# Optimization experiments

Measured on AMD Instinct MI355X. Metric: run time of the kernel, lower is better.

## Reference

```python
import jax, jax.numpy as jnp
import numpy as np

BN_EPS = 1e-5


def setup_inputs() -> dict:
    key = jax.random.key(0)
    ks = jax.random.split(key, 11)
    B, C, Ci, D, H, W = 2, 256, 128, 8, 32, 32
    s = 0.02  # weight init scale
    return {
        "x": jax.random.normal(ks[0], (B, C, D, H, W), dtype=jnp.float32),
        "Wt": jax.random.normal(ks[1], (Ci, C), dtype=jnp.float32) * s,
        "bt": jax.random.normal(ks[2], (Ci,), dtype=jnp.float32) * s,
        "Wp": jax.random.normal(ks[3], (Ci, C), dtype=jnp.float32) * s,
        "bp": jax.random.normal(ks[4], (Ci,), dtype=jnp.float32) * s,
        "Wg": jax.random.normal(ks[5], (Ci, C), dtype=jnp.float32) * s,
        "bg": jax.random.normal(ks[6], (Ci,), dtype=jnp.float32) * s,
        "Ww": jax.random.normal(ks[7], (C, Ci), dtype=jnp.float32) * s,
        "bw": jax.random.normal(ks[8], (C,), dtype=jnp.float32) * s,
        "gamma": jax.random.normal(ks[9], (C,), dtype=jnp.float32),
        "beta": jax.random.normal(ks[10], (C,), dtype=jnp.float32),
    }


def reference(x, Wt, bt, Wp, bp, Wg, bg, Ww, bw, gamma, beta):
    # x: [B, C, D, H, W]; 1x1x1 Conv3d == per-position channel GEMM.
    B, C, D, H, W = x.shape
    xf = x.reshape(B, C, -1)  # [B, C, N], N = D*H*W

    theta = jnp.einsum('oc,bcn->bno', Wt, xf) + bt          # [B, N, Ci]
    phi = jnp.einsum('oc,bcn->bon', Wp, xf) + bp[None, :, None]  # [B, Ci, N]
    g = jnp.einsum('oc,bcn->bno', Wg, xf) + bg              # [B, N, Ci]

    # Unscaled, unmasked full self-attention over all N spatial positions.
    f = jnp.einsum('bnc,bcm->bnm', theta, phi)              # [B, N, N]
    a = jax.nn.softmax(f, axis=-1)
    y = jnp.einsum('bnm,bmc->bcn', a, g)                    # [B, Ci, N]

    # Output projection W: conv1x1 then BatchNorm3d (training-mode batch stats).
    wy = jnp.einsum('oc,bcn->bon', Ww, y) + bw[None, :, None]  # [B, C, N]
    mean = jnp.mean(wy, axis=(0, 2), keepdims=True)
    var = jnp.var(wy, axis=(0, 2), keepdims=True)
    wy_bn = (wy - mean) * jax.lax.rsqrt(var + BN_EPS)
    wy_bn = wy_bn * gamma[None, :, None] + beta[None, :, None]

    return wy_bn.reshape(B, C, D, H, W) + x
```

## Files before the change

### kernel.cpp

```cpp
#include <hip/hip_runtime.h>
#include <cstdint>
#include <cstddef>


typedef unsigned short u16;
typedef __bf16 bf16x8 __attribute__((ext_vector_type(8)));
typedef float f32x4 __attribute__((ext_vector_type(4)));
typedef float f32x16 __attribute__((ext_vector_type(16)));
typedef unsigned short u16x8 __attribute__((ext_vector_type(8)));

#define B_ 2
#define C_ 256
#define CI_ 128
#define N_ 8192
#define CHUNKS 4
#define CHUNK_N 2048
#define KVB 64
#define NT (CHUNK_N/KVB)

static __device__ __forceinline__ u16 f2bf(float f){
  unsigned u = __builtin_bit_cast(unsigned, f);
  unsigned r = (u + 0x7FFFu + ((u>>16)&1u)) >> 16;
  return (u16)r;
}
static __device__ __forceinline__ float bf2f(u16 v){
  unsigned u = ((unsigned)v) << 16;
  return __builtin_bit_cast(float, u);
}
static __device__ __forceinline__ f32x4 f4zero(){
  f32x4 v; v[0]=0.f; v[1]=0.f; v[2]=0.f; v[3]=0.f; return v;
}
static __device__ __forceinline__ f32x16 f16zero(){
  f32x16 v;
#pragma unroll
  for (int i=0;i<16;i++) v[i]=0.f;
  return v;
}
static __device__ __forceinline__ f32x4 mfma16(bf16x8 a, bf16x8 b, f32x4 c){
  return __builtin_amdgcn_mfma_f32_16x16x32_bf16(a, b, c, 0, 0, 0);
}
static __device__ __forceinline__ f32x16 mfma32(bf16x8 a, bf16x8 b, f32x16 c){
  return __builtin_amdgcn_mfma_f32_32x32x16_bf16(a, b, c, 0, 0, 0);
}
static __device__ __forceinline__ unsigned cvtpk(float lo, float hi){
  unsigned r;
  asm("v_cvt_pk_bf16_f32 %0, %1, %2" : "=v"(r) : "v"(lo), "v"(hi));
  return r;
}
static __device__ __forceinline__ void plswap(unsigned &a, unsigned &b){
  asm volatile("v_permlane32_swap_b32 %0, %1" : "+v"(a), "+v"(b));
}

__global__ void k0_prep(const float* __restrict__ Wt, const float* __restrict__ Wp,
                        const float* __restrict__ Wg, const float* __restrict__ Ww,
                        const float* __restrict__ bt, const float* __restrict__ bp,
                        const float* __restrict__ bg,
                        u16* __restrict__ Wcat, u16* __restrict__ Wwb,
                        float* __restrict__ biasc, float* __restrict__ stats){
  int t = blockIdx.x*blockDim.x + threadIdx.x;
  int nthr = gridDim.x*blockDim.x;
  for (int i = t; i < 32768; i += nthr){
    Wcat[i]        = f2bf(Wt[i]);
    Wcat[32768+i]  = f2bf(Wp[i]);
    Wcat[65536+i]  = f2bf(Wg[i]);
    Wwb[i]         = f2bf(Ww[i]);
  }
  for (int i = t; i < 128; i += nthr){
    biasc[i] = bt[i]; biasc[128+i] = bp[i]; biasc[256+i] = bg[i];
  }
  for (int i = t; i < 512; i += nthr) stats[i] = 0.f;
}

__global__ __launch_bounds__(256) void k1_proj(const float* __restrict__ x,
     const u16* __restrict__ Wcat, const float* __restrict__ biasc,
     u16* __restrict__ theta, u16* __restrict__ kproj, u16* __restrict__ gT){
  __shared__ u16 At[64*264];
  __shared__ u16 Wt_[32*264];
  __shared__ u16 gbuf[32*72];
  int tid = threadIdx.x;
  int b  = blockIdx.x >> 7;
  int nb = (blockIdx.x & 127) * 64;
  int w = tid >> 6, lane = tid & 63;
  int l15 = lane & 15, kg = lane >> 4;

  {
    int cp = tid & 127, nh = tid >> 7;
    int c0 = cp*2;
    const float* src0 = x + ((size_t)(b*C_ + c0))*N_ + nb + nh*32;
    const float* src1 = src0 + N_;
#pragma unroll
    for (int j=0;j<8;j++){
      f32x4 a = *(const f32x4*)(src0 + j*4);
      f32x4 c = *(const f32x4*)(src1 + j*4);
#pragma unroll
      for (int q=0;q<4;q++){
        unsigned pk = (unsigned)f2bf(a[q]) | ((unsigned)f2bf(c[q])<<16);
        *(unsigned*)&At[(nh*32 + j*4 + q)*264 + c0] = pk;
      }
    }
  }
  __syncthreads();

  bf16x8 afr[8];
#pragma unroll
  for (int kc=0;kc<8;kc++)
    afr[kc] = *(const bf16x8*)&At[(w*16+l15)*264 + kc*32 + kg*8];

  for (int och = 0; och < 12; och++){
    {
      int o8 = tid>>3, cp8 = tid&7;
      const u16* wsrc = Wcat + ((size_t)(och*32 + o8))*256 + cp8*8;
#pragma unroll
      for (int j=0;j<4;j++)
        *(u16x8*)&Wt_[o8*264 + cp8*8 + j*64] = *(const u16x8*)(wsrc + j*64);
    }
    __syncthreads();

    f32x4 acc0 = f4zero(), acc1 = f4zero();
#pragma unroll
    for (int kc=0;kc<8;kc++){
      bf16x8 b0 = *(const bf16x8*)&Wt_[(l15)*264 + kc*32 + kg*8];
      bf16x8 b1 = *(const bf16x8*)&Wt_[(16+l15)*264 + kc*32 + kg*8];
      acc0 = mfma16(afr[kc], b0, acc0);
      acc1 = mfma16(afr[kc], b1, acc1);
    }

    if (och < 8){
      u16* dst = (och < 4) ? theta : kproj;
      int oo = (och & 3) * 32;
#pragma unroll
      for (int of=0;of<2;of++){
        int o = oo + of*16 + l15;
        float bias = biasc[och*32 + of*16 + l15];
        f32x4 acc = of ? acc1 : acc0;
#pragma unroll
        for (int i=0;i<4;i++){
          int n = nb + w*16 + kg*4 + i;
          dst[((size_t)b*N_ + n)*CI_ + o] = f2bf(acc[i] + bias);
        }
      }
      __syncthreads();
    } else {
#pragma unroll
      for (int of=0;of<2;of++){
        int o = of*16 + l15;
        float bias = biasc[och*32 + of*16 + l15];
        f32x4 acc = of ? acc1 : acc0;
#pragma unroll
        for (int i=0;i<4;i++){
          int r = w*16 + kg*4 + i;
          gbuf[o*72 + r] = f2bf(acc[i] + bias);
        }
      }
      __syncthreads();
      {
        int o = tid>>3, np = tid&7;
        int og = (och-8)*32 + o;
        u16x8 v = *(const u16x8*)&gbuf[o*72 + np*8];
        *(u16x8*)(gT + ((size_t)b*CI_ + og)*N_ + nb + np*8) = v;
      }
      __syncthreads();
    }
  }
}

__global__ __launch_bounds__(512, 2) void k2_attn(const u16* __restrict__ theta,
      const u16* __restrict__ kproj, const u16* __restrict__ gT,
      u16* __restrict__ pO, float* __restrict__ pM, float* __restrict__ pL){
  __shared__ char smem[65536];
  char* kbase = smem;
  char* vbase = smem + 32768;
  int tid = threadIdx.x;
  int bid = blockIdx.x;
  int combo = bid & 7;
  int b = combo & 1;
  int chunk = combo >> 1;
  int qblk = bid >> 3;
  int n0 = chunk * CHUNK_N;
  int w = tid >> 6, lane = tid & 63;
  int l31 = lane & 31, hi = lane >> 5;
  int qg = qblk*256 + w*32 + l31;

  bf16x8 qf[8];
  {
    const u16* qsrc = theta + ((size_t)b*N_ + qg)*CI_ + hi*8;
#pragma unroll
    for (int cc=0; cc<8; cc++) qf[cc] = *(const bf16x8*)(qsrc + cc*16);
  }

  int krow_s = tid >> 3, kpart = tid & 7;
  int vrow_s = tid >> 2, vpart = tid & 3;
  const u16* ksrc = kproj + ((size_t)b*N_ + n0 + krow_s)*CI_ + kpart*16;
  const u16* vsrc = gT + ((size_t)b*CI_ + vrow_s)*N_ + n0 + vpart*16;
  int kw_off[2], vw_off[2];
#pragma unroll
  for (int j=0;j<2;j++){
    int cb = kpart*32 + j*16;
    kw_off[j] = krow_s*256 + (cb ^ ((krow_s&7)<<4));
    int kb = vpart*32 + j*16;
    vw_off[j] = vrow_s*128 + (kb ^ ((vrow_s&7)<<4));
  }
  int swz = (l31&7)<<4;
  int kro[8], vro[4];
#pragma unroll
  for (int cc=0;cc<8;cc++) kro[cc] = l31*256 + ((cc*32 + hi*16) ^ swz);
#pragma unroll
  for (int ks=0;ks<4;ks++) vro[ks] = l31*128 + ((ks*32 + hi*16) ^ swz);

#pragma unroll
  for (int j=0;j<2;j++){
    *(u16x8*)(kbase + kw_off[j]) = *(const u16x8*)(ksrc + j*8);
    *(u16x8*)(vbase + vw_off[j]) = *(const u16x8*)(vsrc + j*8);
  }
  __syncthreads();

  f32x16 oacc[4];
#pragma unroll
  for (int i=0;i<4;i++) oacc[i] = f16zero();
  float mrun = -1e30f, lrun = 0.f;

  for (int t=0; t<NT; t++){
    int cur = t & 1;
    char* kb_c = kbase + cur*16384;
    char* vb_c = vbase + cur*16384;
    u16x8 kst[2], vst[2];
    bool pf = (t+1 < NT);
    if (pf){
      const u16* ks = ksrc + (size_t)(t+1)*KVB*CI_;
      const u16* vs = vsrc + (t+1)*KVB;
#pragma unroll
      for (int j=0;j<2;j++) kst[j] = *(const u16x8*)(ks + j*8);
#pragma unroll
      for (int j=0;j<2;j++) vst[j] = *(const u16x8*)(vs + j*8);
    }

    f32x16 sA = f16zero(), sB = f16zero();
    __builtin_amdgcn_s_setprio(1);
#pragma unroll
    for (int cc=0; cc<8; cc++){
      bf16x8 kf0 = *(const bf16x8*)(kb_c + kro[cc]);
      bf16x8 kf1 = *(const bf16x8*)(kb_c + 8192 + kro[cc]);
      sA = mfma32(kf0, qf[cc], sA);
      sB = mfma32(kf1, qf[cc], sB);
    }
    __builtin_amdgcn_s_setprio(0);

    float t8[8];
#pragma unroll
    for (int i=0;i<8;i++) t8[i] = fmaxf(fmaxf(sA[i], sA[i+8]), fmaxf(sB[i], sB[i+8]));
    float m4a = fmaxf(t8[0], t8[4]), m4b = fmaxf(t8[1], t8[5]);
    float m4c = fmaxf(t8[2], t8[6]), m4d = fmaxf(t8[3], t8[7]);
    float mx = fmaxf(fmaxf(m4a, m4b), fmaxf(m4c, m4d));
    mx = fmaxf(mx, __shfl_xor(mx, 32));
    if (__any(mx > mrun + 8.f)){
      float mnew = fmaxf(mrun, mx);
      float sc = __expf(mrun - mnew);
      lrun *= sc;
#pragma unroll
      for (int i=0;i<4;i++)
#pragma unroll
        for (int r=0;r<16;r++) oacc[i][r] *= sc;
      mrun = mnew;
    }
    float pA[16], pB[16];
#pragma unroll
    for (int r=0;r<16;r++){ pA[r] = __expf(sA[r]-mrun); pB[r] = __expf(sB[r]-mrun); }
    float s8[8];
#pragma unroll
    for (int i=0;i<8;i++) s8[i] = (pA[i]+pA[i+8]) + (pB[i]+pB[i+8]);
    float s4a = s8[0]+s8[4], s4b = s8[1]+s8[5], s4c = s8[2]+s8[6], s4d = s8[3]+s8[7];
    float ps = (s4a+s4b) + (s4c+s4d);
    ps += __shfl_xor(ps, 32);
    lrun += ps;

    if (pf){
      char* kd = kbase + (cur^1)*16384;
      char* vd = vbase + (cur^1)*16384;
#pragma unroll
      for (int j=0;j<2;j++) *(u16x8*)(kd + kw_off[j]) = kst[j];
#pragma unroll
      for (int j=0;j<2;j++) *(u16x8*)(vd + vw_off[j]) = vst[j];
    }

    __builtin_amdgcn_s_setprio(1);
#pragma unroll
    for (int ks=0; ks<4; ks++){
      const float* P = (ks<2) ? pA : pB;
      int r0 = (ks&1)*8;
      unsigned a0 = cvtpk(P[r0+0], P[r0+1]);
      unsigned b0 = cvtpk(P[r0+4], P[r0+5]);
      unsigned a1 = cvtpk(P[r0+2], P[r0+3]);
      unsigned b1 = cvtpk(P[r0+6], P[r0+7]);
      plswap(a0, b0); plswap(a1, b1);
      union { unsigned u[4]; bf16x8 v; } pb;
      pb.u[0]=a0; pb.u[1]=a1; pb.u[2]=b0; pb.u[3]=b1;
#pragma unroll
      for (int c2=0; c2<4; c2++){
        bf16x8 vf = *(const bf16x8*)(vb_c + c2*4096 + vro[ks]);
        oacc[c2] = mfma32(vf, pb.v, oacc[c2]);
      }
    }
    __builtin_amdgcn_s_setprio(0);
    __syncthreads();
  }

  char* region = smem + w*8192;
#pragma unroll
  for (int c2=0;c2<4;c2++)
#pragma unroll
    for (int r=0;r<16;r++){
      int c = c2*32 + (r&3) + 8*(r>>2) + 4*hi;
      *(u16*)(region + l31*256 + ((c*2) ^ swz)) = f2bf(oacc[c2][r]);
    }
  __syncthreads();
  {
    int ql = lane >> 1, half = lane & 1;
    int qg2 = qblk*256 + w*32 + ql;
    u16* dst = pO + ((size_t)(chunk*2 + b)*N_ + qg2)*CI_ + half*64;
    int rswz = (ql&7)<<4;
#pragma unroll
    for (int j=0;j<8;j++){
      u16x8 v2 = *(const u16x8*)(region + ql*256 + ((half*128 + j*16) ^ rswz));
      *(u16x8*)(dst + j*8) = v2;
    }
  }
  if (hi == 0){
    pM[(size_t)(chunk*2 + b)*N_ + qg] = mrun;
    pL[(size_t)(chunk*2 + b)*N_ + qg] = lrun;
  }
}

__global__ __launch_bounds__(256) void k2b_combine(const u16* __restrict__ pO,
    const float* __restrict__ pM, const float* __restrict__ pL,
    float* __restrict__ y){
  int tid = threadIdx.x;
  int blk = blockIdx.x;
  int b = blk >> 9;
  int q = (blk & 511) * 16 + (tid >> 4);
  int c0 = (tid & 15) * 8;
  size_t qi = (size_t)b*N_ + q;
  float m0 = pM[qi], m1 = pM[2*(size_t)N_ + qi], m2 = pM[4*(size_t)N_ + qi], m3 = pM[6*(size_t)N_ + qi];
  float M = fmaxf(fmaxf(m0,m1), fmaxf(m2,m3));
  float w0 = __expf(m0-M), w1 = __expf(m1-M), w2 = __expf(m2-M), w3 = __expf(m3-M);
  float L = w0*pL[qi] + w1*pL[2*(size_t)N_+qi] + w2*pL[4*(size_t)N_+qi] + w3*pL[6*(size_t)N_+qi];
  float inv = 1.f/L;
  float wts[4] = {w0,w1,w2,w3};
  float acc[8];
#pragma unroll
  for (int i=0;i<8;i++) acc[i]=0.f;
  const u16* src = pO + qi*CI_ + c0;
#pragma unroll
  for (int ch=0; ch<4; ch++){
    u16x8 v = *(const u16x8*)(src + (size_t)ch*2*N_*CI_);
#pragma unroll
    for (int i=0;i<8;i++) acc[i] += wts[ch]*bf2f(v[i]);
  }
  float* dst = y + qi*CI_ + c0;
  f32x4 o0, o1;
#pragma unroll
  for (int i=0;i<4;i++){ o0[i] = acc[i]*inv; o1[i] = acc[4+i]*inv; }
  *(f32x4*)dst = o0;
  *(f32x4*)(dst+4) = o1;
}

__global__ __launch_bounds__(256) void k3_wy(const float* __restrict__ y,
    const u16* __restrict__ Wwb, const float* __restrict__ bw,
    float* __restrict__ wy, float* __restrict__ stats){
  __shared__ u16 Yt[64*136];
  __shared__ u16 Wt_[64*136];
  __shared__ float wyb[64*72];
  int tid = threadIdx.x;
  int b  = blockIdx.x >> 7;
  int nb = (blockIdx.x & 127) * 64;
  int w = tid>>6, lane = tid&63;
  int l15 = lane&15, kg = lane>>4;

  {
    int n = tid>>2, cp = tid&3;
    const float* src = y + ((size_t)b*N_ + nb + n)*CI_ + cp*32;
#pragma unroll
    for (int j=0;j<8;j++){
      f32x4 v = *(const f32x4*)(src + j*4);
      unsigned p0 = (unsigned)f2bf(v[0]) | ((unsigned)f2bf(v[1])<<16);
      unsigned p1 = (unsigned)f2bf(v[2]) | ((unsigned)f2bf(v[3])<<16);
      *(unsigned*)&Yt[n*136 + cp*32 + j*4]     = p0;
      *(unsigned*)&Yt[n*136 + cp*32 + j*4 + 2] = p1;
    }
  }
  __syncthreads();

  bf16x8 afr[4];
#pragma unroll
  for (int kc=0;kc<4;kc++)
    afr[kc] = *(const bf16x8*)&Yt[(w*16+l15)*136 + kc*32 + kg*8];

  for (int oc=0; oc<4; oc++){
    {
      int o = tid>>2, cp = tid&3;
      const u16* src = Wwb + ((size_t)(oc*64 + o))*CI_ + cp*32;
#pragma unroll
      for (int j=0;j<4;j++)
        *(u16x8*)&Wt_[o*136 + cp*32 + j*8] = *(const u16x8*)(src + j*8);
    }
    __syncthreads();

    f32x4 acc[4];
#pragma unroll
    for (int of=0;of<4;of++) acc[of] = f4zero();
#pragma unroll
    for (int kc=0;kc<4;kc++){
#pragma unroll
      for (int of=0;of<4;of++){
        bf16x8 bfr = *(const bf16x8*)&Wt_[(of*16+l15)*136 + kc*32 + kg*8];
        acc[of] = mfma16(afr[kc], bfr, acc[of]);
      }
    }
#pragma unroll
    for (int of=0;of<4;of++){
#pragma unroll
      for (int i=0;i<4;i++)
        wyb[(of*16+l15)*72 + w*16 + kg*4 + i] = acc[of][i];
    }
    __syncthreads();
    {
      int o = tid>>2, np = tid&3;
      int og = oc*64 + o;
      float bias = bw[og];
      float sm = 0.f, sq = 0.f;
      float* dst = wy + ((size_t)b*C_ + og)*N_ + nb + np*16;
#pragma unroll
      for (int j=0;j<4;j++){
        f32x4 v;
#pragma unroll
        for (int q=0;q<4;q++){
          float t2 = wyb[o*72 + np*16 + j*4 + q] + bias;
          v[q] = t2; sm += t2; sq += t2*t2;
        }
        *(f32x4*)(dst + j*4) = v;
      }
      sm += __shfl_xor(sm, 1); sm += __shfl_xor(sm, 2);
      sq += __shfl_xor(sq, 1); sq += __shfl_xor(sq, 2);
      if ((tid&3)==0){
        atomicAdd(&stats[og], sm);
        atomicAdd(&stats[256+og], sq);
      }
    }
    __syncthreads();
  }
}

__global__ __launch_bounds__(256) void k4_bn(const float* __restrict__ wy,
    const float* __restrict__ x, const float* __restrict__ stats,
    const float* __restrict__ gamma, const float* __restrict__ beta,
    float* __restrict__ out){
  size_t base = ((size_t)blockIdx.x)*2048 + (size_t)threadIdx.x*8;
  int o = (int)((base >> 13) & 255);
  const float invn = 1.f/16384.f;
  float mean = stats[o]*invn;
  float var  = stats[256+o]*invn - mean*mean;
  float rs = rsqrtf(var + 1e-5f);
  float g = gamma[o]*rs;
  float bb = beta[o];
  f32x4 a0 = *(const f32x4*)(wy + base);
  f32x4 a1 = *(const f32x4*)(wy + base + 4);
  f32x4 x0 = *(const f32x4*)(x + base);
  f32x4 x1 = *(const f32x4*)(x + base + 4);
  f32x4 r0, r1;
#pragma unroll
  for (int q=0;q<4;q++){
    r0[q] = (a0[q]-mean)*g + bb + x0[q];
    r1[q] = (a1[q]-mean)*g + bb + x1[q];
  }
  *(f32x4*)(out + base)     = r0;
  *(f32x4*)(out + base + 4) = r1;
}

extern "C" void kernel_launch(void* const* d_in, const int* in_sizes, int n_in,
                              void* d_out, int out_size, void* d_ws, size_t ws_size,
                              hipStream_t stream){
  const float* x     = (const float*)d_in[0];
  const float* Wt    = (const float*)d_in[1];
  const float* bt    = (const float*)d_in[2];
  const float* Wp    = (const float*)d_in[3];
  const float* bp    = (const float*)d_in[4];
  const float* Wg    = (const float*)d_in[5];
  const float* bg    = (const float*)d_in[6];
  const float* Ww    = (const float*)d_in[7];
  const float* bw    = (const float*)d_in[8];
  const float* gamma = (const float*)d_in[9];
  const float* beta  = (const float*)d_in[10];

  char* ws = (char*)d_ws;
  u16*   theta = (u16*)(ws + 0);
  u16*   kproj = (u16*)(ws + 4194304);
  u16*   gT    = (u16*)(ws + 8388608);
  u16*   pO    = (u16*)(ws + 12582912);
  float* pM    = (float*)(ws + 29360128);
  float* pL    = (float*)(ws + 29622272);
  u16*   Wcat  = (u16*)(ws + 29884416);
  u16*   Wwb   = (u16*)(ws + 30081024);
  float* biasc = (float*)(ws + 30146560);
  float* stats = (float*)(ws + 30148096);
  float* y     = (float*)(ws + 0);
  float* wy    = (float*)(ws + 12582912);
  float* out   = (float*)d_out;

  k0_prep<<<64, 256, 0, stream>>>(Wt, Wp, Wg, Ww, bt, bp, bg, Wcat, Wwb, biasc, stats);
  k1_proj<<<256, 256, 0, stream>>>(x, Wcat, biasc, theta, kproj, gT);
  k2_attn<<<256, 512, 0, stream>>>(theta, kproj, gT, pO, pM, pL);
  k2b_combine<<<1024, 256, 0, stream>>>(pO, pM, pL, y);
  k3_wy<<<256, 256, 0, stream>>>(y, Wwb, bw, wy, stats);
  k4_bn<<<2048, 256, 0, stream>>>(wy, x, stats, gamma, beta, out);
}
```

Baseline: 144.2 us.

## Fuse split-KV combine into output projection, use exp2 softmax, bf16 wy

```diff
diff --git a/kernel.cpp b/kernel.cpp
--- a/kernel.cpp
+++ b/kernel.cpp
@@ -13,10 +13,7 @@
 #define C_ 256
 #define CI_ 128
 #define N_ 8192
-#define CHUNKS 4
-#define CHUNK_N 2048
 #define KVB 64
-#define NT (CHUNK_N/KVB)
 
 static __device__ __forceinline__ u16 f2bf(float f){
   unsigned u = __builtin_bit_cast(unsigned, f);
@@ -50,6 +47,8 @@
 static __device__ __forceinline__ void plswap(unsigned &a, unsigned &b){
   asm volatile("v_permlane32_swap_b32 %0, %1" : "+v"(a), "+v"(b));
 }
+
+#define LOG2E 1.4426950408889634f
 
 __global__ void k0_prep(const float* __restrict__ Wt, const float* __restrict__ Wp,
                         const float* __restrict__ Wg, const float* __restrict__ Ww,
@@ -60,13 +59,13 @@
   int t = blockIdx.x*blockDim.x + threadIdx.x;
   int nthr = gridDim.x*blockDim.x;
   for (int i = t; i < 32768; i += nthr){
-    Wcat[i]        = f2bf(Wt[i]);
+    Wcat[i]        = f2bf(Wt[i] * LOG2E);
     Wcat[32768+i]  = f2bf(Wp[i]);
     Wcat[65536+i]  = f2bf(Wg[i]);
     Wwb[i]         = f2bf(Ww[i]);
   }
   for (int i = t; i < 128; i += nthr){
-    biasc[i] = bt[i]; biasc[128+i] = bp[i]; biasc[256+i] = bg[i];
+    biasc[i] = bt[i] * LOG2E; biasc[128+i] = bp[i]; biasc[256+i] = bg[i];
   }
   for (int i = t; i < 512; i += nthr) stats[i] = 0.f;
 }
@@ -164,9 +163,11 @@
   }
 }
 
-__global__ __launch_bounds__(512, 2) void k2_attn(const u16* __restrict__ theta,
+__global__ __launch_bounds__(256, 2) void k2_attn(const u16* __restrict__ theta,
       const u16* __restrict__ kproj, const u16* __restrict__ gT,
       u16* __restrict__ pO, float* __restrict__ pM, float* __restrict__ pL){
+  constexpr int CHUNK_N = 2048;
+  constexpr int NTI = CHUNK_N / KVB;
   __shared__ char smem[65536];
   char* kbase = smem;
   char* vbase = smem + 32768;
@@ -179,7 +180,7 @@
   int n0 = chunk * CHUNK_N;
   int w = tid >> 6, lane = tid & 63;
   int l31 = lane & 31, hi = lane >> 5;
-  int qg = qblk*256 + w*32 + l31;
+  int qg = qblk*128 + w*32 + l31;
 
   bf16x8 qf[8];
   {
@@ -188,17 +189,15 @@
     for (int cc=0; cc<8; cc++) qf[cc] = *(const bf16x8*)(qsrc + cc*16);
   }
 
-  int krow_s = tid >> 3, kpart = tid & 7;
-  int vrow_s = tid >> 2, vpart = tid & 3;
-  const u16* ksrc = kproj + ((size_t)b*N_ + n0 + krow_s)*CI_ + kpart*16;
-  const u16* vsrc = gT + ((size_t)b*CI_ + vrow_s)*N_ + n0 + vpart*16;
-  int kw_off[2], vw_off[2];
-#pragma unroll
-  for (int j=0;j<2;j++){
-    int cb = kpart*32 + j*16;
-    kw_off[j] = krow_s*256 + (cb ^ ((krow_s&7)<<4));
-    int kb = vpart*32 + j*16;
-    vw_off[j] = vrow_s*128 + (kb ^ ((vrow_s&7)<<4));
+  int krow_s = tid >> 2, kpart = tid & 3;
+  int vrow_s = tid >> 1, vpart = tid & 1;
+  const u16* ksrc = kproj + ((size_t)b*N_ + n0 + krow_s)*CI_ + kpart*32;
+  const u16* vsrc = gT + ((size_t)b*CI_ + vrow_s)*N_ + n0 + vpart*32;
+  int kw_off[4], vw_off[4];
+#pragma unroll
+  for (int j=0;j<4;j++){
+    kw_off[j] = krow_s*256 + ((kpart*64 + j*16) ^ ((krow_s&7)<<4));
+    vw_off[j] = vrow_s*128 + ((vpart*64 + j*16) ^ ((vrow_s&7)<<4));
   }
   int swz = (l31&7)<<4;
   int kro[8], vro[4];
@@ -208,10 +207,9 @@
   for (int ks=0;ks<4;ks++) vro[ks] = l31*128 + ((ks*32 + hi*16) ^ swz);
 
 #pragma unroll
-  for (int j=0;j<2;j++){
-    *(u16x8*)(kbase + kw_off[j]) = *(const u16x8*)(ksrc + j*8);
-    *(u16x8*)(vbase + vw_off[j]) = *(const u16x8*)(vsrc + j*8);
-  }
+  for (int j=0;j<4;j++) *(u16x8*)(kbase + kw_off[j]) = *(const u16x8*)(ksrc + j*8);
+#pragma unroll
+  for (int j=0;j<4;j++) *(u16x8*)(vbase + vw_off[j]) = *(const u16x8*)(vsrc + j*8);
   __syncthreads();
 
   f32x16 oacc[4];
@@ -219,19 +217,19 @@
   for (int i=0;i<4;i++) oacc[i] = f16zero();
   float mrun = -1e30f, lrun = 0.f;
 
-  for (int t=0; t<NT; t++){
+  for (int t=0; t<NTI; t++){
     int cur = t & 1;
     char* kb_c = kbase + cur*16384;
     char* vb_c = vbase + cur*16384;
-    u16x8 kst[2], vst[2];
-    bool pf = (t+1 < NT);
+    u16x8 kst[4], vst[4];
+    bool pf = (t+1 < NTI);
     if (pf){
       const u16* ks = ksrc + (size_t)(t+1)*KVB*CI_;
       const u16* vs = vsrc + (t+1)*KVB;
 #pragma unroll
-      for (int j=0;j<2;j++) kst[j] = *(const u16x8*)(ks + j*8);
-#pragma unroll
-      for (int j=0;j<2;j++) vst[j] = *(const u16x8*)(vs + j*8);
+      for (int j=0;j<4;j++) kst[j] = *(const u16x8*)(ks + j*8);
+#pragma unroll
+      for (int j=0;j<4;j++) vst[j] = *(const u16x8*)(vs + j*8);
     }
 
     f32x16 sA = f16zero(), sB = f16zero();
@@ -252,9 +250,9 @@
     float m4c = fmaxf(t8[2], t8[6]), m4d = fmaxf(t8[3], t8[7]);
     float mx = fmaxf(fmaxf(m4a, m4b), fmaxf(m4c, m4d));
     mx = fmaxf(mx, __shfl_xor(mx, 32));
-    if (__any(mx > mrun + 8.f)){
+    if (__any(mx > mrun + 12.f)){
       float mnew = fmaxf(mrun, mx);
-      float sc = __expf(mrun - mnew);
+      float sc = exp2f(mrun - mnew);
       lrun *= sc;
 #pragma unroll
       for (int i=0;i<4;i++)
@@ -264,7 +262,7 @@
     }
     float pA[16], pB[16];
 #pragma unroll
-    for (int r=0;r<16;r++){ pA[r] = __expf(sA[r]-mrun); pB[r] = __expf(sB[r]-mrun); }
+    for (int r=0;r<16;r++){ pA[r] = exp2f(sA[r]-mrun); pB[r] = exp2f(sB[r]-mrun); }
     float s8[8];
 #pragma unroll
     for (int i=0;i<8;i++) s8[i] = (pA[i]+pA[i+8]) + (pB[i]+pB[i+8]);
@@ -277,9 +275,9 @@
       char* kd = kbase + (cur^1)*16384;
       char* vd = vbase + (cur^1)*16384;
 #pragma unroll
-      for (int j=0;j<2;j++) *(u16x8*)(kd + kw_off[j]) = kst[j];
-#pragma unroll
-      for (int j=0;j<2;j++) *(u16x8*)(vd + vw_off[j]) = vst[j];
+      for (int j=0;j<4;j++) *(u16x8*)(kd + kw_off[j]) = kst[j];
+#pragma unroll
+      for (int j=0;j<4;j++) *(u16x8*)(vd + vw_off[j]) = vst[j];
     }
 
     __builtin_amdgcn_s_setprio(1);
@@ -315,7 +313,7 @@
   __syncthreads();
   {
     int ql = lane >> 1, half = lane & 1;
-    int qg2 = qblk*256 + w*32 + ql;
+    int qg2 = qblk*128 + w*32 + ql;
     u16* dst = pO + ((size_t)(chunk*2 + b)*N_ + qg2)*CI_ + half*64;
     int rswz = (ql&7)<<4;
 #pragma unroll
@@ -330,42 +328,10 @@
   }
 }
 
-__global__ __launch_bounds__(256) void k2b_combine(const u16* __restrict__ pO,
+__global__ __launch_bounds__(256) void k3_wy(const u16* __restrict__ pO,
     const float* __restrict__ pM, const float* __restrict__ pL,
-    float* __restrict__ y){
-  int tid = threadIdx.x;
-  int blk = blockIdx.x;
-  int b = blk >> 9;
-  int q = (blk & 511) * 16 + (tid >> 4);
-  int c0 = (tid & 15) * 8;
-  size_t qi = (size_t)b*N_ + q;
-  float m0 = pM[qi], m1 = pM[2*(size_t)N_ + qi], m2 = pM[4*(size_t)N_ + qi], m3 = pM[6*(size_t)N_ + qi];
-  float M = fmaxf(fmaxf(m0,m1), fmaxf(m2,m3));
-  float w0 = __expf(m0-M), w1 = __expf(m1-M), w2 = __expf(m2-M), w3 = __expf(m3-M);
-  float L = w0*pL[qi] + w1*pL[2*(size_t)N_+qi] + w2*pL[4*(size_t)N_+qi] + w3*pL[6*(size_t)N_+qi];
-  float inv = 1.f/L;
-  float wts[4] = {w0,w1,w2,w3};
-  float acc[8];
-#pragma unroll
-  for (int i=0;i<8;i++) acc[i]=0.f;
-  const u16* src = pO + qi*CI_ + c0;
-#pragma unroll
-  for (int ch=0; ch<4; ch++){
-    u16x8 v = *(const u16x8*)(src + (size_t)ch*2*N_*CI_);
-#pragma unroll
-    for (int i=0;i<8;i++) acc[i] += wts[ch]*bf2f(v[i]);
-  }
-  float* dst = y + qi*CI_ + c0;
-  f32x4 o0, o1;
-#pragma unroll
-  for (int i=0;i<4;i++){ o0[i] = acc[i]*inv; o1[i] = acc[4+i]*inv; }
-  *(f32x4*)dst = o0;
-  *(f32x4*)(dst+4) = o1;
-}
-
-__global__ __launch_bounds__(256) void k3_wy(const float* __restrict__ y,
     const u16* __restrict__ Wwb, const float* __restrict__ bw,
-    float* __restrict__ wy, float* __restrict__ stats){
+    u16* __restrict__ wy, float* __restrict__ stats){
   __shared__ u16 Yt[64*136];
   __shared__ u16 Wt_[64*136];
   __shared__ float wyb[64*72];
@@ -377,14 +343,35 @@
 
   {
     int n = tid>>2, cp = tid&3;
-    const float* src = y + ((size_t)b*N_ + nb + n)*CI_ + cp*32;
-#pragma unroll
-    for (int j=0;j<8;j++){
-      f32x4 v = *(const f32x4*)(src + j*4);
-      unsigned p0 = (unsigned)f2bf(v[0]) | ((unsigned)f2bf(v[1])<<16);
-      unsigned p1 = (unsigned)f2bf(v[2]) | ((unsigned)f2bf(v[3])<<16);
-      *(unsigned*)&Yt[n*136 + cp*32 + j*4]     = p0;
-      *(unsigned*)&Yt[n*136 + cp*32 + j*4 + 2] = p1;
+    size_t q = (size_t)nb + n;
+    float m[4], l[4];
+#pragma unroll
+    for (int ch=0; ch<4; ch++){
+      m[ch] = pM[(size_t)(ch*2+b)*N_ + q];
+      l[ch] = pL[(size_t)(ch*2+b)*N_ + q];
+    }
+    float M = fmaxf(fmaxf(m[0],m[1]), fmaxf(m[2],m[3]));
+    float wts[4]; float L = 0.f;
+#pragma unroll
+    for (int ch=0; ch<4; ch++){ wts[ch] = exp2f(m[ch]-M); L += wts[ch]*l[ch]; }
+    float inv = 1.f/L;
+#pragma unroll
+    for (int j=0;j<4;j++){
+      int c0 = cp*32 + j*8;
+      float acc[8];
+#pragma unroll
+      for (int i=0;i<8;i++) acc[i]=0.f;
+#pragma unroll
+      for (int ch=0; ch<4; ch++){
+        u16x8 v = *(const u16x8*)(pO + ((size_t)(ch*2+b)*N_ + q)*CI_ + c0);
+#pragma unroll
+        for (int i=0;i<8;i++) acc[i] += wts[ch]*bf2f(v[i]);
+      }
+#pragma unroll
+      for (int i=0;i<4;i++){
+        unsigned pk = (unsigned)f2bf(acc[2*i]*inv) | ((unsigned)f2bf(acc[2*i+1]*inv)<<16);
+        *(unsigned*)&Yt[n*136 + c0 + 2*i] = pk;
+      }
     }
   }
   __syncthreads();
@@ -427,17 +414,18 @@
       int og = oc*64 + o;
       float bias = bw[og];
       float sm = 0.f, sq = 0.f;
-      float* dst = wy + ((size_t)b*C_ + og)*N_ + nb + np*16;
+      u16* dst = wy + ((size_t)b*C_ + og)*N_ + nb + np*16;
+      u16 buf[16];
 #pragma unroll
       for (int j=0;j<4;j++){
-        f32x4 v;
-#pragma unroll
-        for (int q=0;q<4;q++){
-          float t2 = wyb[o*72 + np*16 + j*4 + q] + bias;
-          v[q] = t2; sm += t2; sq += t2*t2;
+#pragma unroll
+        for (int q2=0;q2<4;q2++){
+          float t2 = wyb[o*72 + np*16 + j*4 + q2] + bias;
+          buf[j*4+q2] = f2bf(t2); sm += t2; sq += t2*t2;
         }
-        *(f32x4*)(dst + j*4) = v;
-      }
+      }
+      *(u16x8*)dst = *(const u16x8*)&buf[0];
+      *(u16x8*)(dst+8) = *(const u16x8*)&buf[8];
       sm += __shfl_xor(sm, 1); sm += __shfl_xor(sm, 2);
       sq += __shfl_xor(sq, 1); sq += __shfl_xor(sq, 2);
       if ((tid&3)==0){
@@ -449,7 +437,7 @@
   }
 }
 
-__global__ __launch_bounds__(256) void k4_bn(const float* __restrict__ wy,
+__global__ __launch_bounds__(256) void k4_bn(const u16* __restrict__ wy,
     const float* __restrict__ x, const float* __restrict__ stats,
     const float* __restrict__ gamma, const float* __restrict__ beta,
     float* __restrict__ out){
@@ -461,15 +449,14 @@
   float rs = rsqrtf(var + 1e-5f);
   float g = gamma[o]*rs;
   float bb = beta[o];
-  f32x4 a0 = *(const f32x4*)(wy + base);
-  f32x4 a1 = *(const f32x4*)(wy + base + 4);
+  u16x8 a = *(const u16x8*)(wy + base);
   f32x4 x0 = *(const f32x4*)(x + base);
   f32x4 x1 = *(const f32x4*)(x + base + 4);
   f32x4 r0, r1;
 #pragma unroll
   for (int q=0;q<4;q++){
-    r0[q] = (a0[q]-mean)*g + bb + x0[q];
-    r1[q] = (a1[q]-mean)*g + bb + x1[q];
+    r0[q] = (bf2f(a[q])-mean)*g + bb + x0[q];
+    r1[q] = (bf2f(a[4+q])-mean)*g + bb + x1[q];
   }
   *(f32x4*)(out + base)     = r0;
   *(f32x4*)(out + base + 4) = r1;
@@ -497,18 +484,16 @@
   u16*   pO    = (u16*)(ws + 12582912);
   float* pM    = (float*)(ws + 29360128);
   float* pL    = (float*)(ws + 29622272);
-  u16*   Wcat  = (u16*)(ws + 29884416);
-  u16*   Wwb   = (u16*)(ws + 30081024);
-  float* biasc = (float*)(ws + 30146560);
-  float* stats = (float*)(ws + 30148096);
-  float* y     = (float*)(ws + 0);
-  float* wy    = (float*)(ws + 12582912);
+  u16*   wy    = (u16*)(ws + 29884416);
+  u16*   Wcat  = (u16*)(ws + 38273024);
+  u16*   Wwb   = (u16*)(ws + 38469632);
+  float* biasc = (float*)(ws + 38535168);
+  float* stats = (float*)(ws + 38536704);
   float* out   = (float*)d_out;
 
   k0_prep<<<64, 256, 0, stream>>>(Wt, Wp, Wg, Ww, bt, bp, bg, Wcat, Wwb, biasc, stats);
   k1_proj<<<256, 256, 0, stream>>>(x, Wcat, biasc, theta, kproj, gT);
-  k2_attn<<<256, 512, 0, stream>>>(theta, kproj, gT, pO, pM, pL);
-  k2b_combine<<<1024, 256, 0, stream>>>(pO, pM, pL, y);
-  k3_wy<<<256, 256, 0, stream>>>(y, Wwb, bw, wy, stats);
+  k2_attn<<<512, 256, 0, stream>>>(theta, kproj, gT, pO, pM, pL);
+  k3_wy<<<256, 256, 0, stream>>>(pO, pM, pL, Wwb, bw, wy, stats);
   k4_bn<<<2048, 256, 0, stream>>>(wy, x, stats, gamma, beta, out);
 }
```

New measurement: 145.6 us. Within noise of the previous version (+1.0%).
